# Performance work log

Measured on AMD Instinct MI355X. Metric: run time of the kernel, lower is better.

## Reference

```python
import jax, jax.numpy as jnp
import numpy as np


def setup_inputs() -> dict:
    key = jax.random.key(0)
    k1, k2, k3 = jax.random.split(key, 3)
    B, S, D = 8, 2048, 1024
    lstm_output = jax.random.normal(k1, (B, S, D), dtype=jnp.float32)
    W = jax.random.normal(k2, (D, D), dtype=jnp.float32) * (1.0 / np.sqrt(D))
    b = jax.random.normal(k3, (D,), dtype=jnp.float32) * 0.01
    return {"lstm_output": lstm_output, "W": W, "b": b}


def reference(lstm_output, W, b):
    # proj(x) = x @ W^T + b  (torch nn.Linear convention: W is [out, in])
    proj = jnp.einsum('bsd,ed->bse', lstm_output, W) + b          # [B,S,D]
    # scores[b,i,j] = x[b,i] . proj[b,j]
    attn_scores = jnp.einsum('bid,bjd->bij', lstm_output, proj)   # [B,S,S]
    attn_weights = jax.nn.softmax(attn_scores, axis=-1)           # [B,S,S]
    context_vector = jnp.einsum('bij,bjd->bid', attn_weights, lstm_output)
    return (context_vector, attn_weights)
```

## Files before the change

### kernel.cpp

```cpp
#include <hip/hip_runtime.h>


typedef _Float16 f16;
typedef _Float16 f16x8 __attribute__((ext_vector_type(8)));
typedef _Float16 f16x4 __attribute__((ext_vector_type(4)));
typedef float f32x4 __attribute__((ext_vector_type(4)));
typedef unsigned int u32;

#define AS1 __attribute__((address_space(1)))
#define AS3 __attribute__((address_space(3)))

#define FENCE() asm volatile("" ::: "memory")
#define BARRIER()                  \
  do {                             \
    FENCE();                       \
    __builtin_amdgcn_s_barrier();  \
    FENCE();                       \
  } while (0)

static constexpr int Bb = 8, Ss = 2048, Dd = 1024;

__global__ __launch_bounds__(256) void split_cast_k(
    const float* __restrict__ in, f16* __restrict__ hi, f16* __restrict__ lo,
    size_t n4) {
  size_t i = (size_t)blockIdx.x * 256 + threadIdx.x;
  if (i >= n4) return;
  float4 v = ((const float4*)in)[i];
  f16x4 h, l;
  h[0] = (f16)v.x; l[0] = (f16)(v.x - (float)h[0]);
  h[1] = (f16)v.y; l[1] = (f16)(v.y - (float)h[1]);
  h[2] = (f16)v.z; l[2] = (f16)(v.z - (float)h[2]);
  h[3] = (f16)v.w; l[3] = (f16)(v.w - (float)h[3]);
  ((f16x4*)hi)[i] = h;
  ((f16x4*)lo)[i] = l;
}

__global__ __launch_bounds__(256) void cast_k(const float* __restrict__ in,
                                              f16* __restrict__ out,
                                              size_t n4) {
  size_t i = (size_t)blockIdx.x * 256 + threadIdx.x;
  if (i >= n4) return;
  float4 v = ((const float4*)in)[i];
  f16x4 h;
  h[0] = (f16)v.x; h[1] = (f16)v.y; h[2] = (f16)v.z; h[3] = (f16)v.w;
  ((f16x4*)out)[i] = h;
}

__global__ __launch_bounds__(256) void transpose_cast_k(
    const float* __restrict__ x, f16* __restrict__ xT) {
  __shared__ f16 tile[32][33];
  const int b = blockIdx.z;
  const int s0 = blockIdx.x * 32, d0 = blockIdx.y * 32;
  const int tx = threadIdx.x & 31, ty = threadIdx.x >> 5;
  const float* xb = x + (size_t)b * Ss * Dd;
#pragma unroll
  for (int r = 0; r < 32; r += 8)
    tile[ty + r][tx] = (f16)xb[(size_t)(s0 + ty + r) * Dd + d0 + tx];
  __syncthreads();
  f16* xTb = xT + (size_t)b * Dd * Ss;
#pragma unroll
  for (int r = 0; r < 32; r += 8)
    xTb[(size_t)(d0 + ty + r) * Ss + s0 + tx] = tile[tx][ty + r];
}

template <int PPW>
__device__ __forceinline__ void stage_tile(const f16* __restrict__ g,
                                           size_t ld, f16* lds, int wave,
                                           int lane) {
#pragma unroll
  for (int c = 0; c < PPW; ++c) {
    int panel = wave * PPW + c;
    const f16* gp =
        g + (size_t)(panel * 16 + (lane & 15)) * ld + (lane >> 4) * 8;
    AS3 u32* lp = (AS3 u32*)(lds + panel * 512);
    __builtin_amdgcn_global_load_lds((const AS1 u32*)gp, lp, 16, 0, 0);
  }
}

template <bool DUAL_A, bool OUT_F16>
__global__ __launch_bounds__(512, 2) void gemm_bt(
    const f16* __restrict__ A0, const f16* __restrict__ A1,
    const f16* __restrict__ B0, float* __restrict__ C, f16* __restrict__ Ch,
    const float* __restrict__ bias, int K, size_t ldc, size_t sA, size_t sB,
    size_t sC) {
  extern __shared__ f16 smem[];
  const int tid = threadIdx.x;
  const int wave = tid >> 6, lane = tid & 63;
  const size_t tn = (size_t)blockIdx.x * 256;
  const size_t tm = (size_t)blockIdx.y * 256;
  const int b = blockIdx.z;

  constexpr int STAGE = (DUAL_A ? 3 : 2) * 8192;
  constexpr int BOFF = DUAL_A ? 16384 : 8192;

  const f16* Ah = A0 + (size_t)b * sA + tm * (size_t)K;
  const f16* Al = DUAL_A ? (A1 + (size_t)b * sA + tm * (size_t)K) : nullptr;
  const f16* Bp = B0 + (size_t)b * sB + tn * (size_t)K;

  const int wr = wave >> 1, wc = wave & 1;
  const int pA = wr * 4;
  const int pB = wc * 8;

  f16* b0 = smem;
  f16* b1 = smem + STAGE;
  f16* b2 = smem + 2 * STAGE;

  auto stageA = [&](int k, f16* buf) {
    stage_tile<2>(Ah + k, K, buf, wave, lane);
    if constexpr (DUAL_A) stage_tile<2>(Al + k, K, buf + 8192, wave, lane);
  };
  auto stageB = [&](int k, f16* buf) {
    stage_tile<2>(Bp + k, K, buf + BOFF, wave, lane);
  };

  f32x4 acc[4][8] = {};

  const int nIter = K / 32;
  stageA(0, b0); stageB(0, b0);
  stageA(32, b1); stageB(32, b1);
  for (int it = 0; it < nIter; ++it) {
    if (it < nIter - 1) {
      if constexpr (DUAL_A)
        asm volatile("s_waitcnt vmcnt(6)" ::: "memory");
      else
        asm volatile("s_waitcnt vmcnt(4)" ::: "memory");
    } else {
      asm volatile("s_waitcnt vmcnt(0)" ::: "memory");
    }
    BARRIER();

    f16x8 ah[4], al[4], bf[4];
#pragma unroll
    for (int i = 0; i < 4; ++i)
      ah[i] = *(const f16x8*)&b0[(pA + i) * 512 + lane * 8];
#pragma unroll
    for (int j = 0; j < 4; ++j)
      bf[j] = *(const f16x8*)&b0[BOFF + (pB + j) * 512 + lane * 8];
    if constexpr (DUAL_A) {
#pragma unroll
      for (int i = 0; i < 4; ++i)
        al[i] = *(const f16x8*)&b0[8192 + (pA + i) * 512 + lane * 8];
    }
    if (it + 2 < nIter) stageA((it + 2) * 32, b2);
    BARRIER();
    __builtin_amdgcn_s_setprio(1);
#pragma unroll
    for (int j = 0; j < 4; ++j)
#pragma unroll
      for (int i = 0; i < 4; ++i)
        acc[i][j] =
            __builtin_amdgcn_mfma_f32_16x16x32_f16(ah[i], bf[j], acc[i][j], 0, 0, 0);
    if constexpr (DUAL_A) {
#pragma unroll
      for (int j = 0; j < 4; ++j)
#pragma unroll
        for (int i = 0; i < 4; ++i)
          acc[i][j] = __builtin_amdgcn_mfma_f32_16x16x32_f16(al[i], bf[j],
                                                             acc[i][j], 0, 0, 0);
    }
    __builtin_amdgcn_s_setprio(0);

    BARRIER();
    f16x8 bg[4];
#pragma unroll
    for (int j = 0; j < 4; ++j)
      bg[j] = *(const f16x8*)&b0[BOFF + (pB + 4 + j) * 512 + lane * 8];
    if (it + 2 < nIter) stageB((it + 2) * 32, b2);
    BARRIER();
    __builtin_amdgcn_s_setprio(1);
#pragma unroll
    for (int j = 0; j < 4; ++j)
#pragma unroll
      for (int i = 0; i < 4; ++i)
        acc[i][4 + j] = __builtin_amdgcn_mfma_f32_16x16x32_f16(
            ah[i], bg[j], acc[i][4 + j], 0, 0, 0);
    if constexpr (DUAL_A) {
#pragma unroll
      for (int j = 0; j < 4; ++j)
#pragma unroll
        for (int i = 0; i < 4; ++i)
          acc[i][4 + j] = __builtin_amdgcn_mfma_f32_16x16x32_f16(
              al[i], bg[j], acc[i][4 + j], 0, 0, 0);
    }
    __builtin_amdgcn_s_setprio(0);

    f16* t = b0; b0 = b1; b1 = b2; b2 = t;
  }

  const int wm = wr * 64, wn = wc * 128;
#pragma unroll
  for (int i = 0; i < 4; ++i) {
    size_t row0 = tm + wm + i * 16 + ((lane >> 4) << 2);
#pragma unroll
    for (int j = 0; j < 8; ++j) {
      size_t col = tn + wn + j * 16 + (lane & 15);
      float bj = bias ? bias[col] : 0.f;
#pragma unroll
      for (int r = 0; r < 4; ++r) {
        float v = acc[i][j][r] + bj;
        size_t off = (size_t)b * sC + (row0 + r) * ldc + col;
        if constexpr (OUT_F16)
          Ch[off] = (f16)v;
        else
          C[off] = v;
      }
    }
  }
}

__global__ __launch_bounds__(256) void softmax_k(float* __restrict__ sc,
                                                 f16* __restrict__ wh) {
  const size_t row = blockIdx.x;
  float* p = sc + row * 2048;
  f16* w = wh + row * 2048;
  const int t = threadIdx.x;
  float4 v0 = ((const float4*)p)[t];
  float4 v1 = ((const float4*)p)[256 + t];
  float m = fmaxf(fmaxf(fmaxf(v0.x, v0.y), fmaxf(v0.z, v0.w)),
                  fmaxf(fmaxf(v1.x, v1.y), fmaxf(v1.z, v1.w)));
#pragma unroll
  for (int o = 32; o; o >>= 1) m = fmaxf(m, __shfl_xor(m, o, 64));
  __shared__ float red[4];
  if ((t & 63) == 0) red[t >> 6] = m;
  __syncthreads();
  m = fmaxf(fmaxf(red[0], red[1]), fmaxf(red[2], red[3]));
  v0.x = __expf(v0.x - m);
  v0.y = __expf(v0.y - m);
  v0.z = __expf(v0.z - m);
  v0.w = __expf(v0.w - m);
  v1.x = __expf(v1.x - m);
  v1.y = __expf(v1.y - m);
  v1.z = __expf(v1.z - m);
  v1.w = __expf(v1.w - m);
  float s = v0.x + v0.y + v0.z + v0.w + v1.x + v1.y + v1.z + v1.w;
#pragma unroll
  for (int o = 32; o; o >>= 1) s += __shfl_xor(s, o, 64);
  __shared__ float red2[4];
  if ((t & 63) == 0) red2[t >> 6] = s;
  __syncthreads();
  s = red2[0] + red2[1] + red2[2] + red2[3];
  float inv = 1.0f / s;
  v0.x *= inv; v0.y *= inv; v0.z *= inv; v0.w *= inv;
  v1.x *= inv; v1.y *= inv; v1.z *= inv; v1.w *= inv;
  ((float4*)p)[t] = v0;
  ((float4*)p)[256 + t] = v1;
  f16x4 h0, h1;
  h0[0] = (f16)v0.x; h0[1] = (f16)v0.y; h0[2] = (f16)v0.z; h0[3] = (f16)v0.w;
  h1[0] = (f16)v1.x; h1[1] = (f16)v1.y; h1[2] = (f16)v1.z; h1[3] = (f16)v1.w;
  ((f16x4*)w)[t] = h0;
  ((f16x4*)w)[256 + t] = h1;
}

extern "C" void kernel_launch(void* const* d_in, const int* in_sizes, int n_in,
                              void* d_out, int out_size, void* d_ws,
                              size_t ws_size, hipStream_t stream) {
  (void)in_sizes; (void)n_in; (void)out_size; (void)ws_size;
  const float* x = (const float*)d_in[0];
  const float* W = (const float*)d_in[1];
  const float* bias = (const float*)d_in[2];
  float* ctx = (float*)d_out;
  float* scores = (float*)d_out + (size_t)Bb * Ss * Dd;

  const size_t nBSD = (size_t)Bb * Ss * Dd;
  const size_t nDD = (size_t)Dd * Dd;

  f16* p = (f16*)d_ws;
  f16* x_hi = p; p += nBSD;
  f16* x_lo = p; p += nBSD;
  f16* xT   = p; p += nBSD;
  f16* W_hi = p; p += nDD;
  f16* p_hi = p; p += nBSD;
  f16* attnw = x_hi;

  static bool attr_done = false;
  if (!attr_done) {
    hipFuncSetAttribute(reinterpret_cast<const void*>(&gemm_bt<true, true>),
                        hipFuncAttributeMaxDynamicSharedMemorySize, 147456);
    hipFuncSetAttribute(reinterpret_cast<const void*>(&gemm_bt<true, false>),
                        hipFuncAttributeMaxDynamicSharedMemorySize, 147456);
    hipFuncSetAttribute(reinterpret_cast<const void*>(&gemm_bt<false, false>),
                        hipFuncAttributeMaxDynamicSharedMemorySize, 147456);
    attr_done = true;
  }
  constexpr unsigned LDS_DUAL = 3u * 24576u * 2u;
  constexpr unsigned LDS_SINGLE = 3u * 16384u * 2u;

  split_cast_k<<<(unsigned)(nBSD / 4 / 256), 256, 0, stream>>>(x, x_hi, x_lo,
                                                               nBSD / 4);
  cast_k<<<(unsigned)(nDD / 4 / 256), 256, 0, stream>>>(W, W_hi, nDD / 4);
  transpose_cast_k<<<dim3(Ss / 32, Dd / 32, Bb), 256, 0, stream>>>(x, xT);

  gemm_bt<true, true>
      <<<dim3(Dd / 256, (Bb * Ss) / 256, 1), 512, LDS_DUAL, stream>>>(
          x_hi, x_lo, W_hi, nullptr, p_hi, bias, Dd, (size_t)Dd, 0, 0, 0);

  gemm_bt<true, false>
      <<<dim3(Ss / 256, Ss / 256, Bb), 512, LDS_DUAL, stream>>>(
          x_hi, x_lo, p_hi, scores, nullptr, nullptr, Dd, (size_t)Ss,
          (size_t)Ss * Dd, (size_t)Ss * Dd, (size_t)Ss * Ss);

  softmax_k<<<Bb * Ss, 256, 0, stream>>>(scores, attnw);

  gemm_bt<false, false>
      <<<dim3(Dd / 256, Ss / 256, Bb), 512, LDS_SINGLE, stream>>>(
          attnw, nullptr, xT, ctx, nullptr, nullptr, Ss, (size_t)Dd,
          (size_t)Ss * Ss, (size_t)Dd * Ss, (size_t)Ss * Dd);
}
```

Baseline: 570.9 us.

## Restructure GEMM K-loop to one barrier per step, remap blocks per XCD, vectorize transpose

The GEMM main loop now uses a single barrier per K step. It issues the async global-to-LDS prefetch of the stage two steps ahead, loads all fragments, then runs all MFMAs, and the loop is unrolled by three so buffer pointers are fixed. This replaces the four-barrier split A/B schedule. Block indices are also remapped so consecutive tiles land on the same XCD (8-way interleave), aiming for better L2 reuse. The transpose now reads the already-converted f16 x_hi with 64x64 tiles and vector accesses instead of recasting fp32, which cuts memory traffic. Dropping barriers raises the risk of LDS races if the waitcnt and buffer-rotation reasoning is off.

```diff
diff --git a/kernel.cpp b/kernel.cpp
--- a/kernel.cpp
+++ b/kernel.cpp
@@ -9,14 +9,6 @@
 
 #define AS1 __attribute__((address_space(1)))
 #define AS3 __attribute__((address_space(3)))
-
-#define FENCE() asm volatile("" ::: "memory")
-#define BARRIER()                  \
-  do {                             \
-    FENCE();                       \
-    __builtin_amdgcn_s_barrier();  \
-    FENCE();                       \
-  } while (0)
 
 static constexpr int Bb = 8, Ss = 2048, Dd = 1024;
 
@@ -46,21 +38,27 @@
   ((f16x4*)out)[i] = h;
 }
 
-__global__ __launch_bounds__(256) void transpose_cast_k(
-    const float* __restrict__ x, f16* __restrict__ xT) {
-  __shared__ f16 tile[32][33];
+__global__ __launch_bounds__(256) void transpose_f16_k(
+    const f16* __restrict__ xh, f16* __restrict__ xT) {
+  __shared__ f16 tile[64][72];
   const int b = blockIdx.z;
-  const int s0 = blockIdx.x * 32, d0 = blockIdx.y * 32;
-  const int tx = threadIdx.x & 31, ty = threadIdx.x >> 5;
-  const float* xb = x + (size_t)b * Ss * Dd;
-#pragma unroll
-  for (int r = 0; r < 32; r += 8)
-    tile[ty + r][tx] = (f16)xb[(size_t)(s0 + ty + r) * Dd + d0 + tx];
+  const int s0 = blockIdx.x * 64, d0 = blockIdx.y * 64;
+  const int tx = threadIdx.x & 15, ty = threadIdx.x >> 4;
+  const f16* xb = xh + (size_t)b * Ss * Dd;
+#pragma unroll
+  for (int r = 0; r < 64; r += 16) {
+    f16x4 v = *(const f16x4*)&xb[(size_t)(s0 + ty + r) * Dd + d0 + tx * 4];
+    *(f16x4*)&tile[ty + r][tx * 4] = v;
+  }
   __syncthreads();
   f16* xTb = xT + (size_t)b * Dd * Ss;
 #pragma unroll
-  for (int r = 0; r < 32; r += 8)
-    xTb[(size_t)(d0 + ty + r) * Ss + s0 + tx] = tile[tx][ty + r];
+  for (int r = 0; r < 64; r += 16) {
+    f16x4 o;
+#pragma unroll
+    for (int i = 0; i < 4; ++i) o[i] = tile[tx * 4 + i][ty + r];
+    *(f16x4*)&xTb[(size_t)(d0 + ty + r) * Ss + s0 + tx * 4] = o;
+  }
 }
 
 template <int PPW>
@@ -75,6 +73,75 @@
     AS3 u32* lp = (AS3 u32*)(lds + panel * 512);
     __builtin_amdgcn_global_load_lds((const AS1 u32*)gp, lp, 16, 0, 0);
   }
+}
+
+template <bool DUAL_A>
+__device__ __forceinline__ void k_body(int it, int nIter,
+                                       const f16* __restrict__ Ah,
+                                       const f16* __restrict__ Al,
+                                       const f16* __restrict__ Bp, int K,
+                                       f16* cur, f16* stg, int wave, int lane,
+                                       int pA, int pB, f32x4 (&acc)[4][8]) {
+  constexpr int BOFF = DUAL_A ? 16384 : 8192;
+  if (it < nIter - 1) {
+    if constexpr (DUAL_A)
+      asm volatile("s_waitcnt vmcnt(6)" ::: "memory");
+    else
+      asm volatile("s_waitcnt vmcnt(4)" ::: "memory");
+  } else {
+    asm volatile("s_waitcnt vmcnt(0)" ::: "memory");
+  }
+  __builtin_amdgcn_s_barrier();
+  asm volatile("" ::: "memory");
+  if (it + 2 < nIter) {
+    const int k = (it + 2) * 32;
+    stage_tile<2>(Ah + k, K, stg, wave, lane);
+    if constexpr (DUAL_A) stage_tile<2>(Al + k, K, stg + 8192, wave, lane);
+    stage_tile<2>(Bp + k, K, stg + BOFF, wave, lane);
+  }
+  f16x8 ah[4], al[4], bf[4], bg[4];
+#pragma unroll
+  for (int i = 0; i < 4; ++i)
+    ah[i] = *(const f16x8*)&cur[(pA + i) * 512 + lane * 8];
+  if constexpr (DUAL_A) {
+#pragma unroll
+    for (int i = 0; i < 4; ++i)
+      al[i] = *(const f16x8*)&cur[8192 + (pA + i) * 512 + lane * 8];
+  }
+#pragma unroll
+  for (int j = 0; j < 4; ++j)
+    bf[j] = *(const f16x8*)&cur[BOFF + (pB + j) * 512 + lane * 8];
+#pragma unroll
+  for (int j = 0; j < 4; ++j)
+    bg[j] = *(const f16x8*)&cur[BOFF + (pB + 4 + j) * 512 + lane * 8];
+  __builtin_amdgcn_s_setprio(1);
+#pragma unroll
+  for (int j = 0; j < 4; ++j)
+#pragma unroll
+    for (int i = 0; i < 4; ++i)
+      acc[i][j] = __builtin_amdgcn_mfma_f32_16x16x32_f16(ah[i], bf[j],
+                                                         acc[i][j], 0, 0, 0);
+#pragma unroll
+  for (int j = 0; j < 4; ++j)
+#pragma unroll
+    for (int i = 0; i < 4; ++i)
+      acc[i][4 + j] = __builtin_amdgcn_mfma_f32_16x16x32_f16(
+          ah[i], bg[j], acc[i][4 + j], 0, 0, 0);
+  if constexpr (DUAL_A) {
+#pragma unroll
+    for (int j = 0; j < 4; ++j)
+#pragma unroll
+      for (int i = 0; i < 4; ++i)
+        acc[i][j] = __builtin_amdgcn_mfma_f32_16x16x32_f16(al[i], bf[j],
+                                                           acc[i][j], 0, 0, 0);
+#pragma unroll
+    for (int j = 0; j < 4; ++j)
+#pragma unroll
+      for (int i = 0; i < 4; ++i)
+        acc[i][4 + j] = __builtin_amdgcn_mfma_f32_16x16x32_f16(
+            al[i], bg[j], acc[i][4 + j], 0, 0, 0);
+  }
+  __builtin_amdgcn_s_setprio(0);
 }
 
 template <bool DUAL_A, bool OUT_F16>
@@ -86,9 +153,19 @@
   extern __shared__ f16 smem[];
   const int tid = threadIdx.x;
   const int wave = tid >> 6, lane = tid & 63;
-  const size_t tn = (size_t)blockIdx.x * 256;
-  const size_t tm = (size_t)blockIdx.y * 256;
-  const int b = blockIdx.z;
+
+  const unsigned nx = gridDim.x, ny = gridDim.y, nz = gridDim.z;
+  const unsigned f = blockIdx.x + nx * (blockIdx.y + ny * blockIdx.z);
+  const unsigned q = (nx * ny * nz) >> 3;
+  const unsigned L = (f & 7) * q + (f >> 3);
+  const unsigned bx = L % nx;
+  const unsigned t1 = L / nx;
+  const unsigned by = t1 % ny;
+  const unsigned bz = t1 / ny;
+
+  const size_t tn = (size_t)bx * 256;
+  const size_t tm = (size_t)by * 256;
+  const int b = bz;
 
   constexpr int STAGE = (DUAL_A ? 3 : 2) * 8192;
   constexpr int BOFF = DUAL_A ? 16384 : 8192;
@@ -101,90 +178,33 @@
   const int pA = wr * 4;
   const int pB = wc * 8;
 
-  f16* b0 = smem;
-  f16* b1 = smem + STAGE;
-  f16* b2 = smem + 2 * STAGE;
-
-  auto stageA = [&](int k, f16* buf) {
+  f16* const B0_ = smem;
+  f16* const B1_ = smem + STAGE;
+  f16* const B2_ = smem + 2 * STAGE;
+
+  auto stage_all = [&](int k, f16* buf) {
     stage_tile<2>(Ah + k, K, buf, wave, lane);
     if constexpr (DUAL_A) stage_tile<2>(Al + k, K, buf + 8192, wave, lane);
-  };
-  auto stageB = [&](int k, f16* buf) {
     stage_tile<2>(Bp + k, K, buf + BOFF, wave, lane);
   };
 
   f32x4 acc[4][8] = {};
 
   const int nIter = K / 32;
-  stageA(0, b0); stageB(0, b0);
-  stageA(32, b1); stageB(32, b1);
-  for (int it = 0; it < nIter; ++it) {
-    if (it < nIter - 1) {
-      if constexpr (DUAL_A)
-        asm volatile("s_waitcnt vmcnt(6)" ::: "memory");
-      else
-        asm volatile("s_waitcnt vmcnt(4)" ::: "memory");
-    } else {
-      asm volatile("s_waitcnt vmcnt(0)" ::: "memory");
-    }
-    BARRIER();
-
-    f16x8 ah[4], al[4], bf[4];
-#pragma unroll
-    for (int i = 0; i < 4; ++i)
-      ah[i] = *(const f16x8*)&b0[(pA + i) * 512 + lane * 8];
-#pragma unroll
-    for (int j = 0; j < 4; ++j)
-      bf[j] = *(const f16x8*)&b0[BOFF + (pB + j) * 512 + lane * 8];
-    if constexpr (DUAL_A) {
-#pragma unroll
-      for (int i = 0; i < 4; ++i)
-        al[i] = *(const f16x8*)&b0[8192 + (pA + i) * 512 + lane * 8];
-    }
-    if (it + 2 < nIter) stageA((it + 2) * 32, b2);
-    BARRIER();
-    __builtin_amdgcn_s_setprio(1);
-#pragma unroll
-    for (int j = 0; j < 4; ++j)
-#pragma unroll
-      for (int i = 0; i < 4; ++i)
-        acc[i][j] =
-            __builtin_amdgcn_mfma_f32_16x16x32_f16(ah[i], bf[j], acc[i][j], 0, 0, 0);
-    if constexpr (DUAL_A) {
-#pragma unroll
-      for (int j = 0; j < 4; ++j)
-#pragma unroll
-        for (int i = 0; i < 4; ++i)
-          acc[i][j] = __builtin_amdgcn_mfma_f32_16x16x32_f16(al[i], bf[j],
-                                                             acc[i][j], 0, 0, 0);
-    }
-    __builtin_amdgcn_s_setprio(0);
-
-    BARRIER();
-    f16x8 bg[4];
-#pragma unroll
-    for (int j = 0; j < 4; ++j)
-      bg[j] = *(const f16x8*)&b0[BOFF + (pB + 4 + j) * 512 + lane * 8];
-    if (it + 2 < nIter) stageB((it + 2) * 32, b2);
-    BARRIER();
-    __builtin_amdgcn_s_setprio(1);
-#pragma unroll
-    for (int j = 0; j < 4; ++j)
-#pragma unroll
-      for (int i = 0; i < 4; ++i)
-        acc[i][4 + j] = __builtin_amdgcn_mfma_f32_16x16x32_f16(
-            ah[i], bg[j], acc[i][4 + j], 0, 0, 0);
-    if constexpr (DUAL_A) {
-#pragma unroll
-      for (int j = 0; j < 4; ++j)
-#pragma unroll
-        for (int i = 0; i < 4; ++i)
-          acc[i][4 + j] = __builtin_amdgcn_mfma_f32_16x16x32_f16(
-              al[i], bg[j], acc[i][4 + j], 0, 0, 0);
-    }
-    __builtin_amdgcn_s_setprio(0);
-
-    f16* t = b0; b0 = b1; b1 = b2; b2 = t;
+  stage_all(0, B0_);
+  stage_all(32, B1_);
+  int it = 0;
+  for (; it + 3 <= nIter; it += 3) {
+    k_body<DUAL_A>(it, nIter, Ah, Al, Bp, K, B0_, B2_, wave, lane, pA, pB, acc);
+    k_body<DUAL_A>(it + 1, nIter, Ah, Al, Bp, K, B1_, B0_, wave, lane, pA, pB,
+                   acc);
+    k_body<DUAL_A>(it + 2, nIter, Ah, Al, Bp, K, B2_, B1_, wave, lane, pA, pB,
+                   acc);
+  }
+  for (; it < nIter; ++it) {
+    f16* cur = (it % 3 == 0) ? B0_ : (it % 3 == 1) ? B1_ : B2_;
+    f16* stg = (it % 3 == 0) ? B2_ : (it % 3 == 1) ? B0_ : B1_;
+    k_body<DUAL_A>(it, nIter, Ah, Al, Bp, K, cur, stg, wave, lane, pA, pB, acc);
   }
 
   const int wm = wr * 64, wn = wc * 128;
@@ -288,7 +308,7 @@
   split_cast_k<<<(unsigned)(nBSD / 4 / 256), 256, 0, stream>>>(x, x_hi, x_lo,
                                                                nBSD / 4);
   cast_k<<<(unsigned)(nDD / 4 / 256), 256, 0, stream>>>(W, W_hi, nDD / 4);
-  transpose_cast_k<<<dim3(Ss / 32, Dd / 32, Bb), 256, 0, stream>>>(x, xT);
+  transpose_f16_k<<<dim3(Ss / 64, Dd / 64, Bb), 256, 0, stream>>>(x_hi, xT);
 
   gemm_bt<true, true>
       <<<dim3(Dd / 256, (Bb * Ss) / 256, 1), 512, LDS_DUAL, stream>>>(
```

Measured after the change: 869.0 us. +52.2%, slower.

## Split GEMM prefetch into three interleaved phases and vectorize f16 transpose

Applied to the files above, without the earlier changes.

The GEMM main loop now issues the A-hi, A-lo and B prefetches for stage it+2 in three separate phases. Each phase is interleaved with one MFMA block, so global-to-LDS traffic is spread across more compute and fewer loads are in flight at once. This adds extra barriers per iteration in the dual-A path. The transpose kernel now reads the already-cast f16 x_hi with 64x64 tiles and 4-wide vector loads and stores instead of reading fp32 x, cutting its memory traffic.

```diff
diff --git a/kernel.cpp b/kernel.cpp
--- a/kernel.cpp
+++ b/kernel.cpp
@@ -11,11 +11,11 @@
 #define AS3 __attribute__((address_space(3)))
 
 #define FENCE() asm volatile("" ::: "memory")
-#define BARRIER()                  \
-  do {                             \
-    FENCE();                       \
-    __builtin_amdgcn_s_barrier();  \
-    FENCE();                       \
+#define BARRIER()                 \
+  do {                            \
+    FENCE();                      \
+    __builtin_amdgcn_s_barrier(); \
+    FENCE();                      \
   } while (0)
 
 static constexpr int Bb = 8, Ss = 2048, Dd = 1024;
@@ -46,21 +46,27 @@
   ((f16x4*)out)[i] = h;
 }
 
-__global__ __launch_bounds__(256) void transpose_cast_k(
-    const float* __restrict__ x, f16* __restrict__ xT) {
-  __shared__ f16 tile[32][33];
+__global__ __launch_bounds__(256) void transpose_f16_k(
+    const f16* __restrict__ xh, f16* __restrict__ xT) {
+  __shared__ f16 tile[64][72];
   const int b = blockIdx.z;
-  const int s0 = blockIdx.x * 32, d0 = blockIdx.y * 32;
-  const int tx = threadIdx.x & 31, ty = threadIdx.x >> 5;
-  const float* xb = x + (size_t)b * Ss * Dd;
-#pragma unroll
-  for (int r = 0; r < 32; r += 8)
-    tile[ty + r][tx] = (f16)xb[(size_t)(s0 + ty + r) * Dd + d0 + tx];
+  const int s0 = blockIdx.x * 64, d0 = blockIdx.y * 64;
+  const int tx = threadIdx.x & 15, ty = threadIdx.x >> 4;
+  const f16* xb = xh + (size_t)b * Ss * Dd;
+#pragma unroll
+  for (int r = 0; r < 64; r += 16) {
+    f16x4 v = *(const f16x4*)&xb[(size_t)(s0 + ty + r) * Dd + d0 + tx * 4];
+    *(f16x4*)&tile[ty + r][tx * 4] = v;
+  }
   __syncthreads();
   f16* xTb = xT + (size_t)b * Dd * Ss;
 #pragma unroll
-  for (int r = 0; r < 32; r += 8)
-    xTb[(size_t)(d0 + ty + r) * Ss + s0 + tx] = tile[tx][ty + r];
+  for (int r = 0; r < 64; r += 16) {
+    f16x4 o;
+#pragma unroll
+    for (int i = 0; i < 4; ++i) o[i] = tile[tx * 4 + i][ty + r];
+    *(f16x4*)&xTb[(size_t)(d0 + ty + r) * Ss + s0 + tx * 4] = o;
+  }
 }
 
 template <int PPW>
@@ -105,20 +111,20 @@
   f16* b1 = smem + STAGE;
   f16* b2 = smem + 2 * STAGE;
 
-  auto stageA = [&](int k, f16* buf) {
+  auto stage_all = [&](int k, f16* buf) {
     stage_tile<2>(Ah + k, K, buf, wave, lane);
     if constexpr (DUAL_A) stage_tile<2>(Al + k, K, buf + 8192, wave, lane);
-  };
-  auto stageB = [&](int k, f16* buf) {
     stage_tile<2>(Bp + k, K, buf + BOFF, wave, lane);
   };
 
   f32x4 acc[4][8] = {};
 
   const int nIter = K / 32;
-  stageA(0, b0); stageB(0, b0);
-  stageA(32, b1); stageB(32, b1);
+  stage_all(0, b0);
+  stage_all(32, b1);
   for (int it = 0; it < nIter; ++it) {
+    const bool pf = (it + 2 < nIter);
+    const int kpf = (it + 2) * 32;
     if (it < nIter - 1) {
       if constexpr (DUAL_A)
         asm volatile("s_waitcnt vmcnt(6)" ::: "memory");
@@ -129,43 +135,32 @@
     }
     BARRIER();
 
-    f16x8 ah[4], al[4], bf[4];
+    f16x8 ah[4], al[4], bf[4], bg[4];
+
 #pragma unroll
     for (int i = 0; i < 4; ++i)
       ah[i] = *(const f16x8*)&b0[(pA + i) * 512 + lane * 8];
 #pragma unroll
     for (int j = 0; j < 4; ++j)
       bf[j] = *(const f16x8*)&b0[BOFF + (pB + j) * 512 + lane * 8];
-    if constexpr (DUAL_A) {
+    if (pf) stage_tile<2>(Ah + kpf, K, b2, wave, lane);
+    BARRIER();
+    __builtin_amdgcn_s_setprio(1);
+#pragma unroll
+    for (int j = 0; j < 4; ++j)
 #pragma unroll
       for (int i = 0; i < 4; ++i)
-        al[i] = *(const f16x8*)&b0[8192 + (pA + i) * 512 + lane * 8];
-    }
-    if (it + 2 < nIter) stageA((it + 2) * 32, b2);
-    BARRIER();
-    __builtin_amdgcn_s_setprio(1);
-#pragma unroll
-    for (int j = 0; j < 4; ++j)
-#pragma unroll
-      for (int i = 0; i < 4; ++i)
-        acc[i][j] =
-            __builtin_amdgcn_mfma_f32_16x16x32_f16(ah[i], bf[j], acc[i][j], 0, 0, 0);
-    if constexpr (DUAL_A) {
-#pragma unroll
-      for (int j = 0; j < 4; ++j)
-#pragma unroll
-        for (int i = 0; i < 4; ++i)
-          acc[i][j] = __builtin_amdgcn_mfma_f32_16x16x32_f16(al[i], bf[j],
-                                                             acc[i][j], 0, 0, 0);
-    }
+        acc[i][j] = __builtin_amdgcn_mfma_f32_16x16x32_f16(ah[i], bf[j],
+                                                           acc[i][j], 0, 0, 0);
     __builtin_amdgcn_s_setprio(0);
-
-    BARRIER();
-    f16x8 bg[4];
+    BARRIER();
+
 #pragma unroll
     for (int j = 0; j < 4; ++j)
       bg[j] = *(const f16x8*)&b0[BOFF + (pB + 4 + j) * 512 + lane * 8];
-    if (it + 2 < nIter) stageB((it + 2) * 32, b2);
+    if constexpr (DUAL_A) {
+      if (pf) stage_tile<2>(Al + kpf, K, b2 + 8192, wave, lane);
+    }
     BARRIER();
     __builtin_amdgcn_s_setprio(1);
 #pragma unroll
@@ -174,20 +169,41 @@
       for (int i = 0; i < 4; ++i)
         acc[i][4 + j] = __builtin_amdgcn_mfma_f32_16x16x32_f16(
             ah[i], bg[j], acc[i][4 + j], 0, 0, 0);
+    __builtin_amdgcn_s_setprio(0);
+    BARRIER();
+
     if constexpr (DUAL_A) {
+#pragma unroll
+      for (int i = 0; i < 4; ++i)
+        al[i] = *(const f16x8*)&b0[8192 + (pA + i) * 512 + lane * 8];
+    }
+    if (pf) stage_tile<2>(Bp + kpf, K, b2 + BOFF, wave, lane);
+    if constexpr (DUAL_A) {
+      BARRIER();
+      __builtin_amdgcn_s_setprio(1);
+#pragma unroll
+      for (int j = 0; j < 4; ++j)
+#pragma unroll
+        for (int i = 0; i < 4; ++i)
+          acc[i][j] = __builtin_amdgcn_mfma_f32_16x16x32_f16(
+              al[i], bf[j], acc[i][j], 0, 0, 0);
+      __builtin_amdgcn_s_setprio(0);
+      BARRIER();
+
+      __builtin_amdgcn_s_setprio(1);
 #pragma unroll
       for (int j = 0; j < 4; ++j)
 #pragma unroll
         for (int i = 0; i < 4; ++i)
           acc[i][4 + j] = __builtin_amdgcn_mfma_f32_16x16x32_f16(
               al[i], bg[j], acc[i][4 + j], 0, 0, 0);
-    }
-    __builtin_amdgcn_s_setprio(0);
+      __builtin_amdgcn_s_setprio(0);
+    }
 
     f16* t = b0; b0 = b1; b1 = b2; b2 = t;
   }
 
-  const int wm = wr * 64, wn = wc * 128;
+  const int wm = pA * 16, wn = pB * 16;
 #pragma unroll
   for (int i = 0; i < 4; ++i) {
     size_t row0 = tm + wm + i * 16 + ((lane >> 4) << 2);
@@ -288,7 +304,7 @@
   split_cast_k<<<(unsigned)(nBSD / 4 / 256), 256, 0, stream>>>(x, x_hi, x_lo,
                                                                nBSD / 4);
   cast_k<<<(unsigned)(nDD / 4 / 256), 256, 0, stream>>>(W, W_hi, nDD / 4);
-  transpose_cast_k<<<dim3(Ss / 32, Dd / 32, Bb), 256, 0, stream>>>(x, xT);
+  transpose_f16_k<<<dim3(Ss / 64, Dd / 64, Bb), 256, 0, stream>>>(x_hi, xT);
 
   gemm_bt<true, true>
       <<<dim3(Dd / 256, (Bb * Ss) / 256, 1), 512, LDS_DUAL, stream>>>(
```

Result: no change. 574.8 us (+0.7%).
